# Performance work log

Hardware: AMD Instinct MI355X
Metric: run time of the kernel (lower is better)

The kernel has to match this reference:

```python
import jax, jax.numpy as jnp
import numpy as np

B, DIN, DK, DV, H, DOUT = 16384, 2048, 2048, 2048, 16, 512
dk, dv = DK // H, DV // H  # 128, 128

def setup_inputs() -> dict:
    key = jax.random.key(0)
    ks = jax.random.split(key, 10)
    s_in = 1.0 / np.sqrt(DIN)
    s_v = 1.0 / np.sqrt(DV)
    s_2in = 1.0 / np.sqrt(2 * DIN)
    return {
        "x": jax.random.normal(ks[0], (B, DIN), jnp.float32),
        "Wq": jax.random.normal(ks[1], (DIN, DK), jnp.float32) * s_in,
        "Wk": jax.random.normal(ks[2], (DIN, DK), jnp.float32) * s_in,
        "Wv": jax.random.normal(ks[3], (DIN, DV), jnp.float32) * s_in,
        "Wo": jax.random.normal(ks[4], (DV, DIN), jnp.float32) * s_v,
        "bo": jax.random.normal(ks[5], (DIN,), jnp.float32) * s_v,
        "Wg": jax.random.normal(ks[6], (2 * DIN, DIN), jnp.float32) * s_2in,
        "bg": jax.random.normal(ks[7], (DIN,), jnp.float32) * s_2in,
        "Wout": jax.random.normal(ks[8], (DIN, DOUT), jnp.float32) * s_in,
        "bout": jax.random.normal(ks[9], (DOUT,), jnp.float32) * s_in,
    }

def _feat(t):
    # kernel feature map: relu(x) + 1e-4
    return jax.nn.relu(t) + 1e-4

def reference(x, Wq, Wk, Wv, Wo, bo, Wg, bg, Wout, bout):
    b = x.shape[0]
    q = _feat((x @ Wq).reshape(b, H, dk))
    k = _feat((x @ Wk).reshape(b, H, dk))
    v = (x @ Wv).reshape(b, H, dv)
    # linear attention: aggregate over batch (acts as sequence)
    kv = jnp.einsum('bhd,bhe->hde', k, v)            # [H, dk, dv]
    z = 1.0 / (jnp.einsum('bhd,hd->bh', q, k.sum(axis=0)) + 1e-6)  # [B, H]
    att = jnp.einsum('bhd,hde->bhe', q, kv) * z[..., None]         # [B, H, dv]
    att = att.reshape(b, DV)
    out_proj = att @ Wo + bo
    gate = jax.nn.sigmoid(jnp.concatenate([out_proj, x], axis=-1) @ Wg + bg)
    out = gate * out_proj + (1.0 - gate) * x
    return out @ Wout + bout
```

## Files before the change

### kernel.cpp

```cpp
#include <hip/hip_runtime.h>
#include <hip/hip_bf16.h>
#include <math.h>

typedef __bf16 bf16_t;
typedef __attribute__((ext_vector_type(8))) __bf16 bf16x8;
typedef __attribute__((ext_vector_type(4))) __bf16 bf16x4;
typedef __attribute__((ext_vector_type(16))) float f32x16;

#define DEVI __device__ __forceinline__

constexpr int B_SZ = 16384, DIN = 2048, DK = 2048, DV = 2048, NH = 16, DOUT = 512;

DEVI void load_lds16(const void* gptr, void* lptr) {
  __builtin_amdgcn_global_load_lds(
      (const __attribute__((address_space(1))) unsigned int*)gptr,
      (__attribute__((address_space(3))) unsigned int*)lptr,
      16, 0, 0);
}

template <int EPI>
__global__ __launch_bounds__(512, 2) void gemm256(
    const bf16_t* __restrict__ A, int lda, long aZ,
    const bf16_t* __restrict__ Bt, int ldb, long bZ,
    void* __restrict__ Cv, int ldc, long cZ, int K,
    const float* __restrict__ aux1,
    const float* __restrict__ aux2) {
  __shared__ __align__(16) bf16_t lds[2][2][256 * 64];
  const int tid = threadIdx.x;
  const int gx = gridDim.x;
  const int nwg = gx * gridDim.y;
  int flat = blockIdx.y * gx + blockIdx.x;
  flat = (flat & 7) * (nwg >> 3) + (flat >> 3);
  const int bn = flat % gx, bm = flat / gx;
  const int bz = blockIdx.z;

  const int lane = tid & 63, w = tid >> 6;
  const int wr = w >> 2, wc = w & 3;
  const int lm = lane & 31, lh = lane >> 5;

  const bf16_t* __restrict__ Ab = A + (long)bm * 256 * lda + (long)bz * aZ;
  const bf16_t* __restrict__ Bb = Bt + (long)bn * 256 * ldb + (long)bz * bZ;

  const int srow = tid >> 3;
  const int sslot = (tid & 7) ^ (srow & 7);
  const long aOff = (long)srow * lda + sslot * 8;
  const long bOff = (long)srow * ldb + sslot * 8;
  char* const ldsc = (char*)&lds[0][0][0];

  const int xorv = lm & 7;
  const int rbA = (wr * 128 + lm) * 128;
  const int rbB = (wc * 64 + lm) * 128 + 32768;
  int sl16[4];
#pragma unroll
  for (int s = 0; s < 4; ++s) sl16[s] = (((2 * s) | lh) ^ xorv) * 16;

  auto stageA = [&](int buf, int t, int h) {
    const bf16_t* p = Ab + aOff + t * 64 + (long)h * 128 * lda;
    char* d = ldsc + buf * 65536 + h * 16384 + tid * 16;
    load_lds16(p, d);
    load_lds16(p + (long)64 * lda, d + 8192);
  };
  auto stageB = [&](int buf, int t, int h) {
    const bf16_t* p = Bb + bOff + t * 64 + (long)h * 128 * ldb;
    char* d = ldsc + buf * 65536 + 32768 + h * 16384 + tid * 16;
    load_lds16(p, d);
    load_lds16(p + (long)64 * ldb, d + 8192);
  };

  f32x16 acc[4][2] = {};
  const int NT = K >> 6;

  stageA(0, 0, 0); stageA(0, 0, 1); stageB(0, 0, 0); stageB(0, 0, 1);
  if (NT > 1) {
    stageB(1, 1, 0); stageB(1, 1, 1);
    asm volatile("s_waitcnt vmcnt(4)" ::: "memory");
  } else {
    asm volatile("s_waitcnt vmcnt(0)" ::: "memory");
  }
  __builtin_amdgcn_sched_barrier(0);
  __builtin_amdgcn_s_barrier();

  for (int t = 0; t < NT; ++t) {
    const int cur = t & 1;
    const char* base = ldsc + cur * 65536;
    bf16x8 bq[2][4];
#pragma unroll
    for (int m = 0; m < 4; ++m) {
      bf16x8 af[4];
#pragma unroll
      for (int s = 0; s < 4; ++s)
        af[s] = *(const bf16x8*)(base + rbA + m * 4096 + sl16[s]);
      if (m == 0) {
#pragma unroll
        for (int j = 0; j < 2; ++j)
#pragma unroll
          for (int s = 0; s < 4; ++s)
            bq[j][s] = *(const bf16x8*)(base + rbB + j * 4096 + sl16[s]);
      }
      if (m == 0) { if (t + 1 < NT) stageA(cur ^ 1, t + 1, 0); }
      if (m == 1) { if (t + 1 < NT) stageA(cur ^ 1, t + 1, 1); }
      if (m == 2) { if (t + 2 < NT) stageB(cur, t + 2, 0); }
      if (m == 3) { if (t + 2 < NT) stageB(cur, t + 2, 1); }
      __builtin_amdgcn_s_barrier();
      __builtin_amdgcn_s_setprio(1);
#pragma unroll
      for (int s = 0; s < 4; ++s) {
        acc[m][0] = __builtin_amdgcn_mfma_f32_32x32x16_bf16(af[s], bq[0][s], acc[m][0], 0, 0, 0);
        acc[m][1] = __builtin_amdgcn_mfma_f32_32x32x16_bf16(af[s], bq[1][s], acc[m][1], 0, 0, 0);
      }
      __builtin_amdgcn_s_setprio(0);
      if (m == 3) {
        if (t + 2 < NT) asm volatile("s_waitcnt vmcnt(4) lgkmcnt(0)" ::: "memory");
        else            asm volatile("s_waitcnt vmcnt(0) lgkmcnt(0)" ::: "memory");
      } else {
        asm volatile("s_waitcnt lgkmcnt(0)" ::: "memory");
      }
      __builtin_amdgcn_sched_barrier(0);
      __builtin_amdgcn_s_barrier();
    }
  }

#pragma unroll
  for (int i = 0; i < 4; ++i) {
#pragma unroll
    for (int j = 0; j < 2; ++j) {
      const int col = bn * 256 + wc * 64 + j * 32 + lm;
#pragma unroll
      for (int r = 0; r < 16; ++r) {
        const int row = bm * 256 + wr * 128 + i * 32 + (r & 3) + 8 * (r >> 2) + 4 * lh;
        const long cidx = (long)row * ldc + (long)bz * cZ + col;
        float val = acc[i][j][r];
        if (EPI == 0) {
          ((bf16_t*)Cv)[cidx] = (bf16_t)val;
        } else if (EPI == 1) {
          if (col < 4096) val = fmaxf(val, 0.f) + 1e-4f;
          ((bf16_t*)Cv)[cidx] = (bf16_t)val;
        } else if (EPI == 2) {
          val += aux1[col];
          ((bf16_t*)Cv)[cidx] = (bf16_t)val;
        } else if (EPI == 4) {
          const float g = 1.f / (1.f + __expf(-(val + aux1[col])));
          const float op = (float)A[(long)row * lda + col];
          const float xx = aux2[(long)row * DIN + col];
          ((bf16_t*)Cv)[cidx] = (bf16_t)(g * op + (1.f - g) * xx);
        } else if (EPI == 5) {
          ((float*)Cv)[cidx] = val + aux1[col];
        }
      }
    }
  }
}

template <int EPI>
__global__ __launch_bounds__(256, 4) void gemm_bt(
    const bf16_t* __restrict__ A, int lda, long aZ,
    const bf16_t* __restrict__ Bt, int ldb, long bZ,
    void* __restrict__ Cv, int ldc, long cZ, int K,
    const float* __restrict__ aux1,
    const float* __restrict__ aux2) {
  __shared__ __align__(16) bf16_t As[2][128 * 32];
  __shared__ __align__(16) bf16_t Bs[2][128 * 32];
  const int tid = threadIdx.x;
  const int bn = blockIdx.x, bm = blockIdx.y, bz = blockIdx.z;
  const int lane = tid & 63, w = tid >> 6;
  const int wm = (w & 1) * 64, wn = (w >> 1) * 64;
  const int lm = lane & 31, lh = lane >> 5;

  const bf16_t* __restrict__ Ab = A + (long)bm * 128 * lda + (long)bz * aZ;
  const bf16_t* __restrict__ Bb = Bt + (long)bn * 128 * ldb + (long)bz * bZ;

  const int srow = tid >> 2, scol = (tid & 3) * 8;
  const long aRow = (long)srow * lda + scol;
  const long bRow = (long)srow * ldb + scol;

  const char* aBase = (const char*)As + (wm + lm) * 64 + lh * 16;
  const char* bBase = (const char*)Bs + (wn + lm) * 64 + lh * 16;

  f32x16 acc[2][2] = {};

  for (int k0 = 0; k0 < K; k0 += 64) {
    const bf16_t* ap = Ab + aRow + k0;
    const bf16_t* bp = Bb + bRow + k0;
    load_lds16(ap, &As[0][tid * 8]);
    load_lds16(ap + (long)64 * lda, &As[0][2048 + tid * 8]);
    load_lds16(ap + 32, &As[1][tid * 8]);
    load_lds16(ap + (long)64 * lda + 32, &As[1][2048 + tid * 8]);
    load_lds16(bp, &Bs[0][tid * 8]);
    load_lds16(bp + (long)64 * ldb, &Bs[0][2048 + tid * 8]);
    load_lds16(bp + 32, &Bs[1][tid * 8]);
    load_lds16(bp + (long)64 * ldb + 32, &Bs[1][2048 + tid * 8]);
    __syncthreads();
#pragma unroll
    for (int s = 0; s < 4; ++s) {
      const int off = (s >> 1) * 8192 + (s & 1) * 32;
      const bf16x8 af0 = *(const bf16x8*)(aBase + off);
      const bf16x8 af1 = *(const bf16x8*)(aBase + off + 2048);
      const bf16x8 bf0 = *(const bf16x8*)(bBase + off);
      const bf16x8 bf1 = *(const bf16x8*)(bBase + off + 2048);
      acc[0][0] = __builtin_amdgcn_mfma_f32_32x32x16_bf16(af0, bf0, acc[0][0], 0, 0, 0);
      acc[0][1] = __builtin_amdgcn_mfma_f32_32x32x16_bf16(af0, bf1, acc[0][1], 0, 0, 0);
      acc[1][0] = __builtin_amdgcn_mfma_f32_32x32x16_bf16(af1, bf0, acc[1][0], 0, 0, 0);
      acc[1][1] = __builtin_amdgcn_mfma_f32_32x32x16_bf16(af1, bf1, acc[1][1], 0, 0, 0);
    }
    __syncthreads();
  }

#pragma unroll
  for (int i = 0; i < 2; ++i) {
#pragma unroll
    for (int j = 0; j < 2; ++j) {
      const int col = bn * 128 + wn + j * 32 + lm;
#pragma unroll
      for (int r = 0; r < 16; ++r) {
        const int row = bm * 128 + wm + i * 32 + (r & 3) + 8 * (r >> 2) + 4 * lh;
        const long cidx = (long)row * ldc + (long)bz * cZ + col;
        float val = acc[i][j][r];
        if (EPI == 0) {
          ((bf16_t*)Cv)[cidx] = (bf16_t)val;
        } else if (EPI == 5) {
          ((float*)Cv)[cidx] = val + aux1[col];
        }
      }
    }
  }
}

__global__ __launch_bounds__(256) void prep_kernel(
    const float* __restrict__ x, const float* __restrict__ Wq,
    const float* __restrict__ Wk, const float* __restrict__ Wv,
    const float* __restrict__ Wo, const float* __restrict__ Wg,
    const float* __restrict__ Wout, bf16_t* __restrict__ concat,
    bf16_t* __restrict__ WqkvT, bf16_t* __restrict__ WoT,
    bf16_t* __restrict__ WgT, bf16_t* __restrict__ WoutT) {
  const int tid = threadIdx.x;
  int b = blockIdx.x;
  if (b < 32768) {
    const long i = ((long)b * 256 + tid) * 4;
    const long row = i >> 11;
    const int col = (int)(i & 2047);
    const float4 f = *(const float4*)&x[i];
    bf16x4 o;
    o[0] = (bf16_t)f.x; o[1] = (bf16_t)f.y; o[2] = (bf16_t)f.z; o[3] = (bf16_t)f.w;
    *(bf16x4*)&concat[row * 4096 + 2048 + col] = o;
    return;
  }
  b -= 32768;
  const float* in; bf16_t* out; int R, C;
  if (b < 4096)       { in = Wq;   out = WqkvT;                     R = 2048; C = 2048; }
  else if (b < 8192)  { in = Wk;   out = WqkvT + (size_t)2048*2048; R = 2048; C = 2048; b -= 4096; }
  else if (b < 12288) { in = Wv;   out = WqkvT + (size_t)4096*2048; R = 2048; C = 2048; b -= 8192; }
  else if (b < 16384) { in = Wo;   out = WoT;                       R = 2048; C = 2048; b -= 12288; }
  else if (b < 24576) { in = Wg;   out = WgT;                       R = 4096; C = 2048; b -= 16384; }
  else                { in = Wout; out = WoutT;                     R = 2048; C = 512;  b -= 24576; }
  const int CB = C / 32;
  const int c0 = (b % CB) * 32, r0 = (b / CB) * 32;
  __shared__ bf16_t tile[32][33];
  const int tx = tid & 31, ty = tid >> 5;
  for (int i = ty; i < 32; i += 8)
    tile[i][tx] = (bf16_t)in[(long)(r0 + i) * C + c0 + tx];
  __syncthreads();
  for (int i = ty; i < 32; i += 8)
    out[(long)(c0 + i) * R + r0 + tx] = tile[tx][i];
}

__global__ __launch_bounds__(256) void ksum_kernel(const bf16_t* __restrict__ qkv,
                                                   float* __restrict__ ksum) {
  const int col = blockIdx.x * 256 + threadIdx.x;
  const int r0 = blockIdx.y * 256;
  const bf16_t* k = qkv + 2048;
  float s = 0.f;
  for (int r = 0; r < 256; ++r) s += (float)k[(long)(r0 + r) * 6144 + col];
  atomicAdd(&ksum[col], s);
}

__global__ __launch_bounds__(256) void kv_kernel(const bf16_t* __restrict__ qkv,
                                                 float* __restrict__ P) {
  const int h = blockIdx.x, sp = blockIdx.y;
  const int t = threadIdx.x;
  __shared__ __align__(16) bf16_t kS[64 * 128];
  __shared__ __align__(16) bf16_t vS[64 * 128];
  const int d0 = (t >> 4) * 8, e0 = (t & 15) * 8;
  const int srow = t >> 4, scol = (t & 15) * 8;
  float acc[8][8] = {};
  const bf16_t* kp = qkv + 2048 + h * 128;
  const bf16_t* vp = qkv + 4096 + h * 128;
  const long base = (long)sp * 512 * 6144;
  for (int c0 = 0; c0 < 512; c0 += 64) {
#pragma unroll
    for (int it = 0; it < 4; ++it) {
      load_lds16(kp + base + (long)(c0 + it * 16 + srow) * 6144 + scol, &kS[it * 2048 + t * 8]);
      load_lds16(vp + base + (long)(c0 + it * 16 + srow) * 6144 + scol, &vS[it * 2048 + t * 8]);
    }
    __syncthreads();
    for (int bb = 0; bb < 64; ++bb) {
      const bf16x8 kk = *(const bf16x8*)&kS[bb * 128 + d0];
      const bf16x8 vv = *(const bf16x8*)&vS[bb * 128 + e0];
      float kf[8], vf[8];
#pragma unroll
      for (int r = 0; r < 8; ++r) { kf[r] = (float)kk[r]; vf[r] = (float)vv[r]; }
#pragma unroll
      for (int a = 0; a < 8; ++a)
#pragma unroll
        for (int b2 = 0; b2 < 8; ++b2) acc[a][b2] += kf[a] * vf[b2];
    }
    __syncthreads();
  }
  float* Ph = P + (long)h * 16384;
#pragma unroll
  for (int a = 0; a < 8; ++a)
#pragma unroll
    for (int b2 = 0; b2 < 8; ++b2)
      atomicAdd(&Ph[(d0 + a) * 128 + e0 + b2], acc[a][b2]);
}

__global__ __launch_bounds__(256) void cvt_bf(const float* __restrict__ P,
                                              bf16_t* __restrict__ o, int n) {
  const int i = blockIdx.x * 256 + threadIdx.x;
  if (i < n) o[i] = (bf16_t)P[i];
}

__global__ __launch_bounds__(256) void z_kernel(bf16_t* __restrict__ qkv,
                                                const float* __restrict__ ksum) {
  __shared__ float ks[2048];
  const int t = threadIdx.x;
  for (int i = t; i < 2048; i += 256) ks[i] = ksum[i];
  __syncthreads();
  const int b = blockIdx.x * 16 + (t >> 4);
  const int h = t & 15;
  bf16_t* qr = qkv + (long)b * 6144 + h * 128;
  bf16x8 qq[16];
  float s = 0.f;
#pragma unroll
  for (int i = 0; i < 16; ++i) {
    qq[i] = *(const bf16x8*)&qr[i * 8];
#pragma unroll
    for (int r = 0; r < 8; ++r) s += (float)qq[i][r] * ks[h * 128 + i * 8 + r];
  }
  const float z = 1.f / (s + 1e-6f);
#pragma unroll
  for (int i = 0; i < 16; ++i) {
#pragma unroll
    for (int r = 0; r < 8; ++r) qq[i][r] = (bf16_t)((float)qq[i][r] * z);
    *(bf16x8*)&qr[i * 8] = qq[i];
  }
}

extern "C" void kernel_launch(void* const* d_in, const int* in_sizes, int n_in,
                              void* d_out, int out_size, void* d_ws, size_t ws_size,
                              hipStream_t stream) {
  const float* x    = (const float*)d_in[0];
  const float* Wq   = (const float*)d_in[1];
  const float* Wk   = (const float*)d_in[2];
  const float* Wv   = (const float*)d_in[3];
  const float* Wo   = (const float*)d_in[4];
  const float* bo   = (const float*)d_in[5];
  const float* Wg   = (const float*)d_in[6];
  const float* bg   = (const float*)d_in[7];
  const float* Wout = (const float*)d_in[8];
  const float* bout = (const float*)d_in[9];

  char* ws = (char*)d_ws;
  size_t off = 0;
  auto alloc = [&](size_t bytes) -> void* {
    void* p = ws + off;
    off += (bytes + 255) & ~(size_t)255;
    return p;
  };
  bf16_t* concat = (bf16_t*)alloc((size_t)B_SZ * 4096 * 2);
  bf16_t* qkv    = (bf16_t*)alloc((size_t)B_SZ * 6144 * 2);
  bf16_t* outb   = (bf16_t*)alloc((size_t)B_SZ * DIN * 2);
  bf16_t* WqkvT  = (bf16_t*)alloc((size_t)6144 * DIN * 2);
  bf16_t* WoT    = (bf16_t*)alloc((size_t)DIN * DV * 2);
  bf16_t* WgT    = (bf16_t*)alloc((size_t)DIN * 4096 * 2);
  bf16_t* WoutT  = (bf16_t*)alloc((size_t)DOUT * DIN * 2);
  float*  P      = (float*)alloc((size_t)NH * 128 * 128 * 4);
  bf16_t* kvbf   = (bf16_t*)alloc((size_t)NH * 128 * 128 * 2);
  bf16_t* G      = (bf16_t*)alloc((size_t)DIN * DK * 2);
  float*  ksum   = (float*)alloc((size_t)DK * 4);

  hipMemsetAsync(P, 0, (size_t)NH * 128 * 128 * 4, stream);
  hipMemsetAsync(ksum, 0, (size_t)DK * 4, stream);

  prep_kernel<<<32768 + 25600, 256, 0, stream>>>(x, Wq, Wk, Wv, Wo, Wg, Wout,
                                                 concat, WqkvT, WoT, WgT, WoutT);

  const bf16_t* xb = concat + 2048;

  gemm256<1><<<dim3(24, 64, 1), 512, 0, stream>>>(xb, 4096, 0, WqkvT, 2048, 0,
                                                  qkv, 6144, 0, 2048, nullptr, nullptr);

  ksum_kernel<<<dim3(8, 64), 256, 0, stream>>>(qkv, ksum);
  kv_kernel<<<dim3(16, 32), 256, 0, stream>>>(qkv, P);
  cvt_bf<<<1024, 256, 0, stream>>>(P, kvbf, NH * 128 * 128);
  z_kernel<<<B_SZ / 16, 256, 0, stream>>>(qkv, ksum);

  gemm_bt<0><<<dim3(1, 16, 16), 256, 0, stream>>>(WoT, 2048, 128, kvbf, 128, 16384,
                                                  G, 2048, 128, 128, nullptr, nullptr);

  gemm256<2><<<dim3(8, 64, 1), 512, 0, stream>>>(qkv, 6144, 0, G, 2048, 0,
                                                 concat, 4096, 0, 2048, bo, nullptr);

  gemm256<4><<<dim3(8, 64, 1), 512, 0, stream>>>(concat, 4096, 0, WgT, 4096, 0,
                                                 outb, 2048, 0, 4096, bg, x);

  gemm_bt<5><<<dim3(4, 128, 1), 256, 0, stream>>>(outb, 2048, 0, WoutT, 2048, 0,
                                                  d_out, 512, 0, 2048, bout, nullptr);
}
```

Before: 1.569 ms.

## Halve barrier phases per K-tile and refine LDS swizzle for bank conflicts

Restructures the GEMM main loop from four phases per K-tile to two. Each phase now loads two A fragments and issues 16 MFMAs, and the prefetch staging is grouped into one stage per phase. This cuts the number of barriers and waitcnt stalls per tile. The LDS XOR swizzle also mixes in higher row bits on both the store and read sides, aiming to reduce bank conflicts. The trade-off is higher register pressure, since two A fragment sets are live at once, and less interleaving of global loads.

```diff
diff --git a/kernel.cpp b/kernel.cpp
--- a/kernel.cpp
+++ b/kernel.cpp
@@ -42,12 +42,13 @@
   const bf16_t* __restrict__ Bb = Bt + (long)bn * 256 * ldb + (long)bz * bZ;
 
   const int srow = tid >> 3;
-  const int sslot = (tid & 7) ^ (srow & 7);
+  const int fs = (srow & 7) ^ ((srow >> 3) & 3);
+  const int sslot = (tid & 7) ^ fs;
   const long aOff = (long)srow * lda + sslot * 8;
   const long bOff = (long)srow * ldb + sslot * 8;
   char* const ldsc = (char*)&lds[0][0][0];
 
-  const int xorv = lm & 7;
+  const int xorv = (lm & 7) ^ ((lm >> 3) & 3);
   const int rbA = (wr * 128 + lm) * 128;
   const int rbB = (wc * 64 + lm) * 128 + 32768;
   int sl16[4];
@@ -83,41 +84,53 @@
   for (int t = 0; t < NT; ++t) {
     const int cur = t & 1;
     const char* base = ldsc + cur * 65536;
-    bf16x8 bq[2][4];
-#pragma unroll
-    for (int m = 0; m < 4; ++m) {
-      bf16x8 af[4];
+    bf16x8 af[2][4], bq[2][4];
+#pragma unroll
+    for (int s = 0; s < 4; ++s)
+      af[0][s] = *(const bf16x8*)(base + rbA + 0 * 4096 + sl16[s]);
+#pragma unroll
+    for (int j = 0; j < 2; ++j)
 #pragma unroll
       for (int s = 0; s < 4; ++s)
-        af[s] = *(const bf16x8*)(base + rbA + m * 4096 + sl16[s]);
-      if (m == 0) {
-#pragma unroll
-        for (int j = 0; j < 2; ++j)
-#pragma unroll
-          for (int s = 0; s < 4; ++s)
-            bq[j][s] = *(const bf16x8*)(base + rbB + j * 4096 + sl16[s]);
-      }
-      if (m == 0) { if (t + 1 < NT) stageA(cur ^ 1, t + 1, 0); }
-      if (m == 1) { if (t + 1 < NT) stageA(cur ^ 1, t + 1, 1); }
-      if (m == 2) { if (t + 2 < NT) stageB(cur, t + 2, 0); }
-      if (m == 3) { if (t + 2 < NT) stageB(cur, t + 2, 1); }
-      __builtin_amdgcn_s_barrier();
-      __builtin_amdgcn_s_setprio(1);
-#pragma unroll
-      for (int s = 0; s < 4; ++s) {
-        acc[m][0] = __builtin_amdgcn_mfma_f32_32x32x16_bf16(af[s], bq[0][s], acc[m][0], 0, 0, 0);
-        acc[m][1] = __builtin_amdgcn_mfma_f32_32x32x16_bf16(af[s], bq[1][s], acc[m][1], 0, 0, 0);
-      }
-      __builtin_amdgcn_s_setprio(0);
-      if (m == 3) {
-        if (t + 2 < NT) asm volatile("s_waitcnt vmcnt(4) lgkmcnt(0)" ::: "memory");
-        else            asm volatile("s_waitcnt vmcnt(0) lgkmcnt(0)" ::: "memory");
-      } else {
-        asm volatile("s_waitcnt lgkmcnt(0)" ::: "memory");
-      }
-      __builtin_amdgcn_sched_barrier(0);
-      __builtin_amdgcn_s_barrier();
-    }
+        bq[j][s] = *(const bf16x8*)(base + rbB + j * 4096 + sl16[s]);
+#pragma unroll
+    for (int s = 0; s < 4; ++s)
+      af[1][s] = *(const bf16x8*)(base + rbA + 1 * 4096 + sl16[s]);
+    if (t + 1 < NT) { stageA(cur ^ 1, t + 1, 0); stageA(cur ^ 1, t + 1, 1); }
+    __builtin_amdgcn_s_barrier();
+    __builtin_amdgcn_s_setprio(1);
+#pragma unroll
+    for (int s = 0; s < 4; ++s) {
+      acc[0][0] = __builtin_amdgcn_mfma_f32_32x32x16_bf16(af[0][s], bq[0][s], acc[0][0], 0, 0, 0);
+      acc[0][1] = __builtin_amdgcn_mfma_f32_32x32x16_bf16(af[0][s], bq[1][s], acc[0][1], 0, 0, 0);
+      acc[1][0] = __builtin_amdgcn_mfma_f32_32x32x16_bf16(af[1][s], bq[0][s], acc[1][0], 0, 0, 0);
+      acc[1][1] = __builtin_amdgcn_mfma_f32_32x32x16_bf16(af[1][s], bq[1][s], acc[1][1], 0, 0, 0);
+    }
+    __builtin_amdgcn_s_setprio(0);
+    asm volatile("s_waitcnt lgkmcnt(0)" ::: "memory");
+    __builtin_amdgcn_sched_barrier(0);
+    __builtin_amdgcn_s_barrier();
+#pragma unroll
+    for (int s = 0; s < 4; ++s)
+      af[0][s] = *(const bf16x8*)(base + rbA + 2 * 4096 + sl16[s]);
+#pragma unroll
+    for (int s = 0; s < 4; ++s)
+      af[1][s] = *(const bf16x8*)(base + rbA + 3 * 4096 + sl16[s]);
+    if (t + 2 < NT) { stageB(cur, t + 2, 0); stageB(cur, t + 2, 1); }
+    __builtin_amdgcn_s_barrier();
+    __builtin_amdgcn_s_setprio(1);
+#pragma unroll
+    for (int s = 0; s < 4; ++s) {
+      acc[2][0] = __builtin_amdgcn_mfma_f32_32x32x16_bf16(af[0][s], bq[0][s], acc[2][0], 0, 0, 0);
+      acc[2][1] = __builtin_amdgcn_mfma_f32_32x32x16_bf16(af[0][s], bq[1][s], acc[2][1], 0, 0, 0);
+      acc[3][0] = __builtin_amdgcn_mfma_f32_32x32x16_bf16(af[1][s], bq[0][s], acc[3][0], 0, 0, 0);
+      acc[3][1] = __builtin_amdgcn_mfma_f32_32x32x16_bf16(af[1][s], bq[1][s], acc[3][1], 0, 0, 0);
+    }
+    __builtin_amdgcn_s_setprio(0);
+    if (t + 2 < NT) asm volatile("s_waitcnt vmcnt(4) lgkmcnt(0)" ::: "memory");
+    else            asm volatile("s_waitcnt vmcnt(0) lgkmcnt(0)" ::: "memory");
+    __builtin_amdgcn_sched_barrier(0);
+    __builtin_amdgcn_s_barrier();
   }
 
 #pragma unroll
```

New measurement: 1.506 ms. 4.0% less time.
